# Kernel optimization log

Hardware: AMD Instinct MI355X
Metric: run time of the kernel (lower is better)

The kernel has to match this reference:

```python
import jax, jax.numpy as jnp
import numpy as np
from jax import lax

C, NORI, NROT, K, PAD = 256, 8, 2, 3, 1
B, H, W = 16, 64, 64
EPS = 1e-5


def setup_inputs() -> dict:
    key = jax.random.key(0)
    k1, k2, k3 = jax.random.split(key, 3)
    x = jax.random.normal(k1, (B, C, H, W), dtype=jnp.float32)
    # rotate_arf() output: [nRot*C, nOri*C, K, K]
    weight_all = jax.random.normal(k2, (NROT * C, NORI * C, K, K), dtype=jnp.float32) * 0.02
    bias_all = jax.random.normal(k3, (NROT * C,), dtype=jnp.float32) * 0.02
    alpha = jnp.float32(1.0)
    gamma = jnp.ones((C,), dtype=jnp.float32)
    beta = jnp.zeros((C,), dtype=jnp.float32)
    return {"x": x, "weight_all": weight_all, "bias_all": bias_all,
            "alpha": alpha, "gamma": gamma, "beta": beta}


def _forward(x, weight_all, bias_all, alpha, gamma, beta):
    # Loop of nOri*nRot convs over the same x with different weight blocks,
    # all accumulated into one [B,C,H,W] tensor == single conv with summed blocks
    # (conv is linear in the weights): fused form of the original loop.
    W_eff = weight_all.reshape(NROT, C, NORI, C, K, K).sum(axis=(0, 2))  # [C, C, K, K]
    b_eff = bias_all.reshape(NROT, C).sum(axis=0) * NORI                 # [C]
    d_sum = lax.conv_general_dilated(
        x, W_eff, window_strides=(1, 1), padding=[(PAD, PAD), (PAD, PAD)],
        dimension_numbers=("NCHW", "OIHW", "NCHW"))
    d_sum = d_sum + b_eff[None, :, None, None]
    d_mean = d_sum / float(NORI * NROT)
    out = x + alpha * d_mean
    # BatchNorm2d, training mode: biased batch stats over (B, H, W)
    mean = out.mean(axis=(0, 2, 3))
    var = ((out - mean[None, :, None, None]) ** 2).mean(axis=(0, 2, 3))
    inv = lax.rsqrt(var + EPS)
    y = (out - mean[None, :, None, None]) * (gamma * inv)[None, :, None, None] \
        + beta[None, :, None, None]
    return y


def reference(x, weight_all, bias_all, alpha, gamma, beta):
    return _forward(x, weight_all, bias_all, alpha, gamma, beta)
```

## Files before the change

### kernel.cpp

```cpp
#include <hip/hip_runtime.h>
#include <stdint.h>

typedef __attribute__((__ext_vector_type__(8))) __bf16 bf16x8;
typedef __attribute__((__ext_vector_type__(4))) float  f32x4;

#define XT_OFF    0ul
#define WT_OFF    33554432ul
#define BEFF_OFF  34734080ul
#define ZERO_OFF  34737152ul
#define STATS_OFF 34737408ul
#define V_OFF     35651584ul
#define WS_NEED   (V_OFF + 33554432ul)

__device__ inline void gload_lds16(const void* g, void* l) {
  __builtin_amdgcn_global_load_lds((const __attribute__((address_space(1))) void*)g,
                                   (__attribute__((address_space(3))) void*)l,
                                   16, 0, 0);
}

__global__ void k_prep(const float* __restrict__ w, const float* __restrict__ bias,
                       const float* __restrict__ alpha_p, __bf16* __restrict__ Wt,
                       float* __restrict__ beff, float* __restrict__ zerob,
                       float* __restrict__ statsG,
                       const float* __restrict__ x, __bf16* __restrict__ xT) {
  __shared__ __bf16 lds[64 * 258];
  if (blockIdx.x < 256) {
    const int co = blockIdx.x;
    const int ci = threadIdx.x;
    float a[9];
#pragma unroll
    for (int t = 0; t < 9; ++t) a[t] = 0.f;
#pragma unroll
    for (int r = 0; r < 2; ++r)
#pragma unroll
      for (int o = 0; o < 8; ++o) {
        const float* p = w + ((size_t)(r * 256 + co) * 2048 + (size_t)(o * 256 + ci)) * 9;
#pragma unroll
        for (int t = 0; t < 9; ++t) a[t] += p[t];
      }
    const float sc = alpha_p[0] * 0.0625f;
    const int s = ci >> 6, cis = ci & 63;
#pragma unroll
    for (int t = 0; t < 9; ++t)
      Wt[(size_t)(t * 4 + s) * 16384 + co * 64 + cis] = (__bf16)(a[t] * sc);
    if (ci == 0) beff[co] = (bias[co] + bias[256 + co]) * 8.0f * sc;
    if (blockIdx.x == 0) {
      statsG[ci] = 0.f; statsG[256 + ci] = 0.f;
      if (ci < 64) zerob[ci] = 0.f;
    }
  } else {
    int bh = blockIdx.x - 256;
    int b = bh >> 6, h = bh & 63;
    int t = threadIdx.x;
    int w2 = t & 63, cg = t >> 6;
    const float* xb = x + ((size_t)b * 16384 + h) * 64;
#pragma unroll 4
    for (int cb = 0; cb < 256; cb += 4) {
      int ci = cb + cg;
      lds[w2 * 258 + ci] = (__bf16)xb[(size_t)ci * 4096 + w2];
    }
    __syncthreads();
    const uint32_t* l32 = (const uint32_t*)lds;
    uint32_t* o32 = (uint32_t*)(xT + ((size_t)b * 64 + h) * 64 * 256);
    int c2 = t & 127, wg = t >> 7;
    for (int w0 = 0; w0 < 64; w0 += 2) {
      int ww = w0 + wg;
      o32[ww * 128 + c2] = l32[ww * 129 + c2];
    }
  }
}

#define A_BYTES 51200
#define B_BYTES 16384

__global__ __launch_bounds__(512, 4) void k_conv(
    const float* __restrict__ x, const __bf16* __restrict__ xT,
    const __bf16* __restrict__ Wt, const float* __restrict__ beff,
    const __bf16* __restrict__ zerob, float* __restrict__ out,
    float* __restrict__ statsG, __bf16* __restrict__ vout, int use_v16)
{
  __shared__ __align__(16) char lds[A_BYTES + B_BYTES + 1024];
  const int u    = blockIdx.x;
  const int ch   = (u >> 3) & 1;
  const int pairid = (u & 7) | ((u >> 4) << 3);
  const int bb   = pairid >> 4;
  const int ho0  = (pairid & 15) << 2;
  const int tid  = threadIdx.x;
  const int lane = tid & 63;
  const int wid  = tid >> 6;
  const int wr   = wid >> 1;
  const int wc   = wid & 1;
  const int l15  = lane & 15;

  f32x4 acc[4][4];
#pragma unroll
  for (int i = 0; i < 4; ++i)
#pragma unroll
    for (int j = 0; j < 4; ++j)
#pragma unroll
      for (int r = 0; r < 4; ++r) acc[i][j][r] = 0.f;

  const char* zb = (const char*)zerob;

  int boff[4][2];
#pragma unroll
  for (int j = 0; j < 4; ++j)
#pragma unroll
    for (int kk = 0; kk < 2; ++kk) {
      const int col    = (wc << 6) + (j << 4) + l15;
      const int ci_off = (kk << 5) + ((lane >> 4) << 3);
      boff[j][kk] = ((col << 7) + (ci_off << 1)) ^ ((col & 7) << 4);
    }
  const int bl = lane >> 3;
  const int bsrcLane = (bl << 7) + (((lane & 7) ^ (bl & 7)) << 4);

  auto stageA = [&](int s) {
    const int ci0 = s << 6;
    for (int t = wid; t < 50; t += 8) {
      const int chk = (t << 3) + (lane >> 3);
      const int r  = chk / 66;
      const int c  = chk - r * 66;
      const int ir = ho0 - 1 + r;
      const int ic = c - 1;
      const int k  = (lane & 7) ^ (chk & 7);
      const char* src;
      if (chk < 396 && ir >= 0 && ir < 64 && ic >= 0 && ic < 64)
        src = (const char*)(xT + ((((size_t)bb << 6) + ir) * 64 + ic) * 256 + ci0 + (k << 3));
      else
        src = zb + (k << 4);
      gload_lds16(src, lds + (t << 10));
    }
  };

  auto stageB = [&](int ph) {
    char* buf = lds + A_BYTES;
    const int s2 = ph / 9, tp = ph - s2 * 9;
    const char* wsrc = (const char*)Wt + ((size_t)(tp * 4 + s2) << 15) + (ch << 14) + bsrcLane;
    gload_lds16(wsrc + (wid << 10), buf + (wid << 10));
    gload_lds16(wsrc + ((wid + 8) << 10), buf + ((wid + 8) << 10));
  };

  int s = 0, tap = 0;
  for (int p = 0; p < 36; ++p) {
    if (tap == 0) stageA(s);
    stageB(p);
    asm volatile("s_waitcnt vmcnt(0)" ::: "memory");
    __builtin_amdgcn_s_barrier();
    asm volatile("" ::: "memory");

    const int dh = (tap >= 6) ? 2 : (tap >= 3 ? 1 : 0);
    const int dw = tap - dh * 3;
    const char* Bb = lds + A_BYTES;
    __builtin_amdgcn_s_setprio(1);
#pragma unroll
    for (int kk = 0; kk < 2; ++kk) {
      const int ci_off = (kk << 5) + ((lane >> 4) << 3);
      bf16x8 av[4];
#pragma unroll
      for (int i = 0; i < 4; ++i) {
        const int pos = (wr + dh) * 66 + (i << 4) + l15 + dw;
        const int off = ((pos << 7) + (ci_off << 1)) ^ ((pos & 7) << 4);
        av[i] = *(const bf16x8*)(lds + off);
      }
#pragma unroll
      for (int j = 0; j < 4; ++j) {
        const bf16x8 bv = *(const bf16x8*)(Bb + boff[j][kk]);
#pragma unroll
        for (int i = 0; i < 4; ++i)
          acc[i][j] = __builtin_amdgcn_mfma_f32_16x16x32_bf16(av[i], bv, acc[i][j], 0, 0, 0);
      }
    }
    __builtin_amdgcn_s_setprio(0);
    asm volatile("" ::: "memory");
    __builtin_amdgcn_s_barrier();
    asm volatile("" ::: "memory");

    if (++tap == 9) { tap = 0; ++s; }
  }

  __syncthreads();
  float* lstat = (float*)(lds + A_BYTES + B_BYTES);
  if (tid < 256) lstat[tid] = 0.f;
  __syncthreads();

  char* wreg = lds + wid * 2048;
  const int wq = lane >> 4;
  const int ho = ho0 + wr;
  const int xorco = (l15 & 7) << 4;
#pragma unroll
  for (int j = 0; j < 4; ++j) {
    const int col = (wc << 6) + (j << 4) + l15;
    const int cog = (ch << 7) + col;
    const float be = beff[cog];
    const size_t base = ((((size_t)bb << 8) + (size_t)cog) << 12) + (ho << 6);
    float r1 = 0.f, r2 = 0.f;
#pragma unroll
    for (int i = 0; i < 4; ++i) {
      const int w0 = (i << 4) + (wq << 2);
      const float4 xv = *(const float4*)(x + base + w0);
      float4 v;
      v.x = acc[i][j][0] + xv.x + be;
      v.y = acc[i][j][1] + xv.y + be;
      v.z = acc[i][j][2] + xv.z + be;
      v.w = acc[i][j][3] + xv.w + be;
      r1 += v.x + v.y + v.z + v.w;
      r2 += v.x * v.x + v.y * v.y + v.z * v.z + v.w * v.w;
      if (use_v16) {
        union { __bf16 h[4]; uint64_t u64; } pk;
        pk.h[0] = (__bf16)v.x; pk.h[1] = (__bf16)v.y;
        pk.h[2] = (__bf16)v.z; pk.h[3] = (__bf16)v.w;
        const int wa = (l15 << 7) + (i << 5) + (wq << 3);
        *(uint64_t*)(wreg + (wa ^ xorco)) = pk.u64;
      } else {
        *(float4*)(out + base + w0) = v;
      }
    }
    r1 += __shfl_xor(r1, 16); r2 += __shfl_xor(r2, 16);
    r1 += __shfl_xor(r1, 32); r2 += __shfl_xor(r2, 32);
    if (lane < 16) {
      atomicAdd(&lstat[col], r1);
      atomicAdd(&lstat[128 + col], r2);
    }
    if (use_v16) {
      asm volatile("s_waitcnt lgkmcnt(0)" ::: "memory");
#pragma unroll
      for (int t2 = 0; t2 < 2; ++t2) {
        const int co_r = lane >> 2;
        const int chk  = (lane & 3) + (t2 << 2);
        const int ra   = (co_r << 7) + (chk << 4);
        const uint4 pv = *(const uint4*)(wreg + (ra ^ ((co_r & 7) << 4)));
        const int co_g = (ch << 7) + (wc << 6) + (j << 4) + co_r;
        const size_t oi = ((((size_t)bb << 8) + (size_t)co_g) << 12) + (ho << 6) + (chk << 3);
        *(uint4*)(vout + oi) = pv;
      }
      asm volatile("s_waitcnt lgkmcnt(0)" ::: "memory");
    }
  }
  __syncthreads();
  if (tid < 256) {
    const int c = tid & 127, part = tid >> 7;
    atomicAdd(&statsG[part * 256 + (ch << 7) + c], lstat[part * 128 + c]);
  }
}

__global__ void k_apply_v16(const __bf16* __restrict__ v, float* __restrict__ out,
                            const float* __restrict__ statsG,
                            const float* __restrict__ gamma,
                            const float* __restrict__ beta) {
  __shared__ float ssc[256], ssh[256];
  const int t = threadIdx.x;
  {
    const float mean = statsG[t] * (1.f / 65536.f);
    const float var  = statsG[256 + t] * (1.f / 65536.f) - mean * mean;
    const float inv  = rsqrtf(var + 1e-5f);
    const float sc   = gamma[t] * inv;
    ssc[t] = sc;
    ssh[t] = beta[t] - mean * sc;
  }
  __syncthreads();
  const uint4* vp = (const uint4*)v;
  for (size_t g = (size_t)blockIdx.x * 256 + t; g < 2097152ul; g += (size_t)gridDim.x * 256) {
    const int co = (int)((g >> 9) & 255);
    const uint4 pv = vp[g];
    const float sc = ssc[co], sh = ssh[co];
    float4 y0, y1;
    y0.x = __uint_as_float((pv.x & 0xffffu) << 16) * sc + sh;
    y0.y = __uint_as_float(pv.x & 0xffff0000u) * sc + sh;
    y0.z = __uint_as_float((pv.y & 0xffffu) << 16) * sc + sh;
    y0.w = __uint_as_float(pv.y & 0xffff0000u) * sc + sh;
    y1.x = __uint_as_float((pv.z & 0xffffu) << 16) * sc + sh;
    y1.y = __uint_as_float(pv.z & 0xffff0000u) * sc + sh;
    y1.z = __uint_as_float((pv.w & 0xffffu) << 16) * sc + sh;
    y1.w = __uint_as_float(pv.w & 0xffff0000u) * sc + sh;
    float4* op = (float4*)(out + g * 8);
    op[0] = y0;
    op[1] = y1;
  }
}

__global__ void k_apply_f32(float* __restrict__ out, const float* __restrict__ statsG,
                            const float* __restrict__ gamma,
                            const float* __restrict__ beta) {
  __shared__ float ssc[256], ssh[256];
  const int t = threadIdx.x;
  {
    const float mean = statsG[t] * (1.f / 65536.f);
    const float var  = statsG[256 + t] * (1.f / 65536.f) - mean * mean;
    const float inv  = rsqrtf(var + 1e-5f);
    const float sc   = gamma[t] * inv;
    ssc[t] = sc;
    ssh[t] = beta[t] - mean * sc;
  }
  __syncthreads();
  float4* op = (float4*)out;
  for (size_t g = (size_t)blockIdx.x * 256 + t; g < 4194304ul; g += (size_t)gridDim.x * 256) {
    const int co = (int)((g >> 10) & 255);
    float4 y = op[g];
    const float sc = ssc[co], sh = ssh[co];
    y.x = y.x * sc + sh; y.y = y.y * sc + sh;
    y.z = y.z * sc + sh; y.w = y.w * sc + sh;
    op[g] = y;
  }
}

extern "C" void kernel_launch(void* const* d_in, const int* in_sizes, int n_in,
                              void* d_out, int out_size, void* d_ws, size_t ws_size,
                              hipStream_t stream) {
  const float* x     = (const float*)d_in[0];
  const float* wall  = (const float*)d_in[1];
  const float* bias  = (const float*)d_in[2];
  const float* alpha = (const float*)d_in[3];
  const float* gamma = (const float*)d_in[4];
  const float* beta  = (const float*)d_in[5];
  float* out = (float*)d_out;

  char* ws = (char*)d_ws;
  __bf16* xT     = (__bf16*)(ws + XT_OFF);
  __bf16* Wt     = (__bf16*)(ws + WT_OFF);
  float*  beff   = (float*)(ws + BEFF_OFF);
  float*  zerob  = (float*)(ws + ZERO_OFF);
  float*  statsG = (float*)(ws + STATS_OFF);
  __bf16* vbuf   = (__bf16*)(ws + V_OFF);
  const int use_v16 = (ws_size >= WS_NEED) ? 1 : 0;

  k_prep<<<1280, 256, 0, stream>>>(wall, bias, alpha, Wt, beff, zerob, statsG, x, xT);
  k_conv<<<512, 512, 0, stream>>>(x, xT, Wt, beff, (const __bf16*)zerob, out,
                                  statsG, vbuf, use_v16);
  if (use_v16)
    k_apply_v16<<<2048, 256, 0, stream>>>(vbuf, out, statsG, gamma, beta);
  else
    k_apply_f32<<<2048, 256, 0, stream>>>(out, statsG, gamma, beta);
}
```

Before: 115.7 us.

## Double-buffer weight tiles and drop column halo from input LDS tile

Weight (B) tiles are now double-buffered in LDS and prefetched two phases ahead, so loads for later taps overlap the MFMA work on the current one instead of waiting on vmcnt(0) every phase. The input tile is stored without left and right halo columns (64 rather than 66 per row), and border taps clamp the column index and zero the fragment in registers. This frees enough LDS for the second B buffer and removes the division by 66 in staging. The cost is extra select logic in the inner loop, and the stage-A reload at tap 8 now depends on a barrier protocol whose correctness is subtle.

```diff
diff --git a/kernel.cpp b/kernel.cpp
--- a/kernel.cpp
+++ b/kernel.cpp
@@ -70,7 +70,7 @@
   }
 }
 
-#define A_BYTES 51200
+#define A_BYTES 49152
 #define B_BYTES 16384
 
 __global__ __launch_bounds__(512, 4) void k_conv(
@@ -79,7 +79,7 @@
     const __bf16* __restrict__ zerob, float* __restrict__ out,
     float* __restrict__ statsG, __bf16* __restrict__ vout, int use_v16)
 {
-  __shared__ __align__(16) char lds[A_BYTES + B_BYTES + 1024];
+  __shared__ __align__(16) char lds[A_BYTES + 2 * B_BYTES];
   const int u    = blockIdx.x;
   const int ch   = (u >> 3) & 1;
   const int pairid = (u & 7) | ((u >> 4) << 3);
@@ -101,6 +101,7 @@
       for (int r = 0; r < 4; ++r) acc[i][j][r] = 0.f;
 
   const char* zb = (const char*)zerob;
+  const bf16x8 zfrag = {};
 
   int boff[4][2];
 #pragma unroll
@@ -116,52 +117,71 @@
 
   auto stageA = [&](int s) {
     const int ci0 = s << 6;
-    for (int t = wid; t < 50; t += 8) {
+#pragma unroll
+    for (int t2 = 0; t2 < 6; ++t2) {
+      const int t   = wid + (t2 << 3);
       const int chk = (t << 3) + (lane >> 3);
-      const int r  = chk / 66;
-      const int c  = chk - r * 66;
+      const int r  = chk >> 6;
+      const int c  = chk & 63;
       const int ir = ho0 - 1 + r;
-      const int ic = c - 1;
       const int k  = (lane & 7) ^ (chk & 7);
       const char* src;
-      if (chk < 396 && ir >= 0 && ir < 64 && ic >= 0 && ic < 64)
-        src = (const char*)(xT + ((((size_t)bb << 6) + ir) * 64 + ic) * 256 + ci0 + (k << 3));
+      if (ir >= 0 && ir < 64)
+        src = (const char*)(xT + ((((size_t)bb << 6) + ir) * 64 + c) * 256 + ci0 + (k << 3));
       else
         src = zb + (k << 4);
       gload_lds16(src, lds + (t << 10));
     }
   };
 
-  auto stageB = [&](int ph) {
-    char* buf = lds + A_BYTES;
+  auto stageB = [&](int ph, int si) {
+    char* buf = lds + A_BYTES + si * B_BYTES;
     const int s2 = ph / 9, tp = ph - s2 * 9;
     const char* wsrc = (const char*)Wt + ((size_t)(tp * 4 + s2) << 15) + (ch << 14) + bsrcLane;
     gload_lds16(wsrc + (wid << 10), buf + (wid << 10));
     gload_lds16(wsrc + ((wid + 8) << 10), buf + ((wid + 8) << 10));
   };
 
+  stageA(0);
+  stageB(0, 0);
+  stageB(1, 1);
+  asm volatile("s_waitcnt vmcnt(2)" ::: "memory");
+  __builtin_amdgcn_s_barrier();
+  asm volatile("" ::: "memory");
+
   int s = 0, tap = 0;
   for (int p = 0; p < 36; ++p) {
-    if (tap == 0) stageA(s);
-    stageB(p);
-    asm volatile("s_waitcnt vmcnt(0)" ::: "memory");
-    __builtin_amdgcn_s_barrier();
-    asm volatile("" ::: "memory");
-
     const int dh = (tap >= 6) ? 2 : (tap >= 3 ? 1 : 0);
     const int dw = tap - dh * 3;
-    const char* Bb = lds + A_BYTES;
+    const char* Bb = lds + A_BYTES + (p & 1) * B_BYTES;
+    const int bcol = l15 + dw - 1;
+    const int c0 = (bcol < 0) ? 0 : bcol;
+    const int c3r = bcol + 48;
+    const int c3 = (c3r > 63) ? 63 : c3r;
+    const int rowb = (wr + dh) << 6;
+    const bool oob0 = (dw == 0);
+    const bool oob3 = (dw == 2);
     __builtin_amdgcn_s_setprio(1);
 #pragma unroll
     for (int kk = 0; kk < 2; ++kk) {
       const int ci_off = (kk << 5) + ((lane >> 4) << 3);
+      const int cib2 = ci_off << 1;
       bf16x8 av[4];
-#pragma unroll
-      for (int i = 0; i < 4; ++i) {
-        const int pos = (wr + dh) * 66 + (i << 4) + l15 + dw;
-        const int off = ((pos << 7) + (ci_off << 1)) ^ ((pos & 7) << 4);
-        av[i] = *(const bf16x8*)(lds + off);
-      }
+      {
+        const int col = c0;
+        av[0] = *(const bf16x8*)(lds + ((((rowb + col) << 7) + cib2) ^ ((col & 7) << 4)));
+      }
+#pragma unroll
+      for (int i = 1; i < 3; ++i) {
+        const int col = bcol + (i << 4);
+        av[i] = *(const bf16x8*)(lds + ((((rowb + col) << 7) + cib2) ^ ((col & 7) << 4)));
+      }
+      {
+        const int col = c3;
+        av[3] = *(const bf16x8*)(lds + ((((rowb + col) << 7) + cib2) ^ ((col & 7) << 4)));
+      }
+      if (oob0) av[0] = (l15 == 0) ? zfrag : av[0];
+      if (oob3) av[3] = (l15 == 15) ? zfrag : av[3];
 #pragma unroll
       for (int j = 0; j < 4; ++j) {
         const bf16x8 bv = *(const bf16x8*)(Bb + boff[j][kk]);
@@ -175,11 +195,21 @@
     __builtin_amdgcn_s_barrier();
     asm volatile("" ::: "memory");
 
+    if (tap == 8 && s < 3) stageA(s + 1);
+    if (p + 2 < 36) {
+      stageB(p + 2, p & 1);
+      asm volatile("s_waitcnt vmcnt(2)" ::: "memory");
+    } else if (p + 1 < 36) {
+      asm volatile("s_waitcnt vmcnt(0)" ::: "memory");
+    }
+    __builtin_amdgcn_s_barrier();
+    asm volatile("" ::: "memory");
+
     if (++tap == 9) { tap = 0; ++s; }
   }
 
   __syncthreads();
-  float* lstat = (float*)(lds + A_BYTES + B_BYTES);
+  float* lstat = (float*)(lds + A_BYTES);
   if (tid < 256) lstat[tid] = 0.f;
   __syncthreads();
 
```

Measured after the change: 117.5 us. About the same (+1.6%).
